# Optimization experiments

Measured on AMD Instinct MI355X. Metric: run time of the kernel, lower is better.

Reference implementation:

```python
import jax, jax.numpy as jnp
import numpy as np
import math

HEADS = 8

def setup_inputs() -> dict:
    key = jax.random.key(0)
    k1, k2 = jax.random.split(key)
    B, C, H, W = 8, 512, 32, 32
    x = jax.random.normal(k1, (B, C, H, W), dtype=jnp.float32)
    # weight-norm 1x1 conv params: v ~ N(0, 0.05), g initialized to ||v|| (torch weight_norm default)
    proj_v = jax.random.normal(k2, (3 * C, C), dtype=jnp.float32) * 0.05
    proj_g = jnp.linalg.norm(proj_v, axis=1)
    proj_b = jnp.zeros((3 * C,), dtype=jnp.float32)
    return {"x": x, "proj_v": proj_v, "proj_g": proj_g, "proj_b": proj_b}

def reference(x, proj_v, proj_g, proj_b):
    B, C, H, W = x.shape
    heads = HEADS
    dim = C // heads
    N = H * W
    # weight-normalized 1x1 conv: w = g * v / ||v|| per output channel
    w = proj_g[:, None] * proj_v / jnp.linalg.norm(proj_v, axis=1, keepdims=True)
    c = jnp.einsum('oc,bchw->bohw', w, x) + proj_b[None, :, None, None]
    c = c.reshape(B, 3, heads, dim, N)
    q, k, v = c[:, 0], c[:, 1], c[:, 2]  # each (B, heads, dim, N)
    scale = 1.0 / math.sqrt(dim)
    attn = jnp.einsum('bhdq,bhdk->bhqk', q, k) * scale  # (B, heads, N, N)
    attn = jax.nn.softmax(attn, axis=-1)
    out = jnp.einsum('bhdk,bhqk->bhdq', v, attn)  # (B, heads, dim, N)
    return x + out.reshape(B, C, H, W)
```

## Files before the change

kernel.cpp:

```cpp
#include <hip/hip_runtime.h>

typedef _Float16 f16;
typedef _Float16 f16x2 __attribute__((ext_vector_type(2)));
typedef _Float16 f16x4 __attribute__((ext_vector_type(4)));
typedef _Float16 f16x8 __attribute__((ext_vector_type(8)));
typedef float f32x4 __attribute__((ext_vector_type(4)));
typedef float f32x16 __attribute__((ext_vector_type(16)));

__device__ inline f32x16 mfma32(f16x8 a, f16x8 b, f32x16 c) {
    return __builtin_amdgcn_mfma_f32_32x32x16_f16(a, b, c, 0, 0, 0);
}

__device__ inline f16x2 pk2(float a, float b) {
    return __builtin_bit_cast(f16x2, __builtin_amdgcn_cvt_pkrtz(a, b));
}

__device__ inline void st8(f16* p, f16x8 v) {
    *(f16x4*)p = __builtin_shufflevector(v, v, 0, 1, 2, 3);
    *(f16x4*)(p + 4) = __builtin_shufflevector(v, v, 4, 5, 6, 7);
}
__device__ inline f16x8 ld8(const f16* p) {
    f16x4 lo = *(const f16x4*)p;
    f16x4 hi = *(const f16x4*)(p + 4);
    return __builtin_shufflevector(lo, hi, 0, 1, 2, 3, 4, 5, 6, 7);
}

__global__ __launch_bounds__(256) void prep_k(const float* __restrict__ pv,
                                              const float* __restrict__ pg,
                                              f16* __restrict__ w,
                                              const float* __restrict__ x,
                                              f16* __restrict__ xT) {
    int bid = blockIdx.x;
    if (bid < 1536) {
        int o = bid;
        const float* row = pv + (size_t)o * 512;
        float s = 0.f;
        for (int c = threadIdx.x; c < 512; c += 256) { float t = row[c]; s += t * t; }
        for (int off = 32; off; off >>= 1) s += __shfl_down(s, off, 64);
        __shared__ float red[4];
        int lane = threadIdx.x & 63, wid = threadIdx.x >> 6;
        if (lane == 0) red[wid] = s;
        __syncthreads();
        float tot = red[0] + red[1] + red[2] + red[3];
        float scale = pg[o] * rsqrtf(tot);
        for (int c = threadIdx.x; c < 512; c += 256)
            w[(size_t)o * 512 + c] = (f16)(row[c] * scale);
    } else {
        int t2 = bid - 1536;
        int n0 = (t2 & 31) * 32, c0 = ((t2 >> 5) & 15) * 32, b = t2 >> 9;
        int tx = threadIdx.x & 31, ty = threadIdx.x >> 5;
        __shared__ float t[32][33];
        const float* xb = x + (size_t)b * 512 * 1024;
        for (int i = 0; i < 4; i++)
            t[ty + 8 * i][tx] = xb[(size_t)(c0 + ty + 8 * i) * 1024 + n0 + tx];
        __syncthreads();
        f16* xTb = xT + (size_t)b * 1024 * 512;
        for (int i = 0; i < 4; i++)
            xTb[(size_t)(n0 + ty + 8 * i) * 512 + c0 + tx] = (f16)t[tx][ty + 8 * i];
    }
}

__global__ __launch_bounds__(256) void qkv_gemm_k(const f16* __restrict__ w,
                                                  const f16* __restrict__ xT,
                                                  const float* __restrict__ pb,
                                                  f16* __restrict__ qk,
                                                  f16* __restrict__ v) {
    __shared__ f16 lA[128 * 64];
    __shared__ f16 lB[128 * 64];
    int b = blockIdx.z;
    int oBase = blockIdx.y * 128;
    int nBase = blockIdx.x * 128;
    const f16* xb = xT + (size_t)b * 1024 * 512;
    int tid = threadIdx.x, lane = tid & 63, warp = tid >> 6;
    int wy = warp >> 1, wx = warp & 1;
    int l31 = lane & 31, hi = lane >> 5;

    int srow = lane >> 3;
    int phys = lane & 7;
    int schunk = phys ^ srow;
    const f16* aS[4]; const f16* bS[4]; int ldsOff[4];
    for (int j = 0; j < 4; j++) {
        int rb = (warp * 4 + j) * 8;
        aS[j] = w  + (size_t)(oBase + rb + srow) * 512 + schunk * 8;
        bS[j] = xb + (size_t)(nBase + rb + srow) * 512 + schunk * 8;
        ldsOff[j] = (rb + srow) * 64 + phys * 8;
    }
    int phk[4];
    for (int ks = 0; ks < 4; ks++)
        phk[ks] = (((ks * 2 + hi) ^ (l31 & 7))) * 8;

    f16x8 rA[4], rB[4];
    for (int j = 0; j < 4; j++) {
        rA[j] = *(const f16x8*)aS[j];
        rB[j] = *(const f16x8*)bS[j];
    }

    f32x16 acc[2][2] = {};

    for (int i = 0; i < 8; i++) {
        __syncthreads();
        for (int j = 0; j < 4; j++) {
            *(f16x8*)&lA[ldsOff[j]] = rA[j];
            *(f16x8*)&lB[ldsOff[j]] = rB[j];
        }
        __syncthreads();
        if (i < 7) {
            int k0 = (i + 1) * 64;
            for (int j = 0; j < 4; j++) {
                rA[j] = *(const f16x8*)(aS[j] + k0);
                rB[j] = *(const f16x8*)(bS[j] + k0);
            }
        }
        for (int ks = 0; ks < 4; ks++) {
            f16x8 af[2], bf[2];
            for (int mi = 0; mi < 2; mi++)
                af[mi] = *(f16x8*)&lA[(wy * 64 + mi * 32 + l31) * 64 + phk[ks]];
            for (int ni = 0; ni < 2; ni++)
                bf[ni] = *(f16x8*)&lB[(wx * 64 + ni * 32 + l31) * 64 + phk[ks]];
            for (int mi = 0; mi < 2; mi++)
                for (int ni = 0; ni < 2; ni++)
                    acc[mi][ni] = mfma32(af[mi], bf[ni], acc[mi][ni]);
        }
    }

    int selB = oBase >> 9;
    for (int mi = 0; mi < 2; mi++) {
        for (int g = 0; g < 4; g++) {
            int oR = oBase + wy * 64 + mi * 32 + 8 * g + 4 * hi;
            int h = (oR >> 6) & 7, d0 = oR & 63;
            for (int ni = 0; ni < 2; ni++) {
                int n = nBase + wx * 64 + ni * 32 + l31;
                if (selB < 2) {
                    float sc = selB == 0 ? 0.125f : 1.0f;
                    f16x4 o4;
                    for (int r = 0; r < 4; r++)
                        o4[r] = (f16)((acc[mi][ni][g * 4 + r] + pb[oR + r]) * sc);
                    *(f16x4*)&qk[((((size_t)b * 2 + selB) * 8 + h) * 1024 + n) * 64 + d0] = o4;
                } else {
                    for (int r = 0; r < 4; r++) {
                        float val = acc[mi][ni][g * 4 + r] + pb[oR + r];
                        v[(((size_t)b * 8 + h) * 64 + d0 + r) * 1024 + n] = (f16)val;
                    }
                }
            }
        }
    }
}

#define ALDK 68
__global__ __launch_bounds__(256) void attn_k(const f16* __restrict__ qk,
                                              const f16* __restrict__ vg,
                                              const float* __restrict__ x,
                                              float* __restrict__ out) {
    __shared__ __align__(16) f16 smem[(2 * 64 + 4 * 32) * ALDK];
    f16* lK = smem;
    f16* lV = smem + 64 * ALDK;
    f16* lPb = smem + 2 * 64 * ALDK;
    float* OT = (float*)smem;

    int bh = blockIdx.y;
    int b = bh >> 3, h = bh & 7;
    int qBase = blockIdx.x * 128;
    int tid = threadIdx.x, lane = tid & 63, warp = tid >> 6;
    int l31 = lane & 31, hi = lane >> 5;

    const f16* qbase = qk + (((size_t)b * 2 + 0) * 8 + h) * 1024 * 64;
    const f16* kbase = qk + (((size_t)b * 2 + 1) * 8 + h) * 1024 * 64;
    const f16* vbase = vg + ((size_t)b * 8 + h) * 64 * 1024;
    f16* lP = lPb + warp * 32 * ALDK;

    int q0 = qBase + warp * 32;
    f16x8 aq[4];
    for (int ks = 0; ks < 4; ks++)
        aq[ks] = *(const f16x8*)&qbase[(size_t)(q0 + l31) * 64 + ks * 16 + hi * 8];

    int sr0 = tid >> 3, sc0 = (tid & 7) * 8;
    int sr1 = (tid + 256) >> 3, sc1 = sc0;

    f16x8 rK[2], rV[2];
    rK[0] = *(const f16x8*)&kbase[(size_t)sr0 * 64 + sc0];
    rK[1] = *(const f16x8*)&kbase[(size_t)sr1 * 64 + sc1];
    rV[0] = *(const f16x8*)&vbase[(size_t)sr0 * 1024 + sc0];
    rV[1] = *(const f16x8*)&vbase[(size_t)sr1 * 1024 + sc1];

    f32x16 accO[2] = {};
    float l_cur = 0.f;

    for (int kt = 0; kt < 16; kt++) {
        __syncthreads();
        st8(&lK[sr0 * ALDK + sc0], rK[0]);
        st8(&lK[sr1 * ALDK + sc1], rK[1]);
        st8(&lV[sr0 * ALDK + sc0], rV[0]);
        st8(&lV[sr1 * ALDK + sc1], rV[1]);
        __syncthreads();
        if (kt < 15) {
            const f16* kb = kbase + (size_t)(kt + 1) * 64 * 64;
            rK[0] = *(const f16x8*)&kb[(size_t)sr0 * 64 + sc0];
            rK[1] = *(const f16x8*)&kb[(size_t)sr1 * 64 + sc1];
            rV[0] = *(const f16x8*)&vbase[(size_t)sr0 * 1024 + (kt + 1) * 64 + sc0];
            rV[1] = *(const f16x8*)&vbase[(size_t)sr1 * 1024 + (kt + 1) * 64 + sc1];
        }

        f32x16 stt[2] = {};
        for (int mt = 0; mt < 2; mt++)
            for (int ks = 0; ks < 4; ks++) {
                f16x8 ak = ld8(&lK[(mt * 32 + l31) * ALDK + ks * 16 + hi * 8]);
                stt[mt] = mfma32(ak, aq[ks], stt[mt]);
            }

        float rs = 0.f;
        for (int mt = 0; mt < 2; mt++)
            for (int g = 0; g < 4; g++) {
                float p0 = __expf(stt[mt][g * 4 + 0]);
                float p1 = __expf(stt[mt][g * 4 + 1]);
                float p2 = __expf(stt[mt][g * 4 + 2]);
                float p3 = __expf(stt[mt][g * 4 + 3]);
                rs += (p0 + p1) + (p2 + p3);
                f16x2 lo = pk2(p0, p1);
                f16x2 hi2 = pk2(p2, p3);
                f16x4 pk;
                pk[0] = lo[0]; pk[1] = lo[1]; pk[2] = hi2[0]; pk[3] = hi2[1];
                *(f16x4*)&lP[l31 * ALDK + mt * 32 + 8 * g + 4 * hi] = pk;
            }
        rs += __shfl_xor(rs, 32, 64);
        l_cur += rs;

        for (int dt = 0; dt < 2; dt++)
            for (int ks = 0; ks < 4; ks++) {
                f16x8 av = ld8(&lV[(dt * 32 + l31) * ALDK + ks * 16 + hi * 8]);
                f16x8 bp = ld8(&lP[l31 * ALDK + ks * 16 + hi * 8]);
                accO[dt] = mfma32(av, bp, accO[dt]);
            }
    }

    __syncthreads();
    float rl = 1.0f / l_cur;
    for (int dt = 0; dt < 2; dt++)
        for (int g = 0; g < 4; g++)
            for (int r = 0; r < 4; r++)
                OT[(dt * 32 + 8 * g + 4 * hi + r) * 132 + warp * 32 + l31] =
                    accO[dt][g * 4 + r] * rl;
    __syncthreads();
    for (int i = 0; i < 8; i++) {
        int cid = tid + 256 * i;
        int d = cid >> 5, qi = (cid & 31) * 4;
        float4 o4 = *(float4*)&OT[d * 132 + qi];
        size_t gi = ((size_t)b * 512 + h * 64 + d) * 1024 + qBase + qi;
        float4 xv = *(const float4*)&x[gi];
        o4.x += xv.x; o4.y += xv.y; o4.z += xv.z; o4.w += xv.w;
        *(float4*)&out[gi] = o4;
    }
}

extern "C" void kernel_launch(void* const* d_in, const int* in_sizes, int n_in,
                              void* d_out, int out_size, void* d_ws, size_t ws_size,
                              hipStream_t stream) {
    (void)in_sizes; (void)n_in; (void)out_size; (void)ws_size;
    const float* x  = (const float*)d_in[0];
    const float* pv = (const float*)d_in[1];
    const float* pg = (const float*)d_in[2];
    const float* pb = (const float*)d_in[3];
    float* out = (float*)d_out;

    char* ws = (char*)d_ws;
    f16* w   = (f16*)(ws);
    f16* xT  = (f16*)(ws + 1572864);
    f16* qk  = (f16*)(ws + 1572864 + 8388608);
    f16* v   = (f16*)(ws + 1572864 + 8388608 + 16777216);

    hipLaunchKernelGGL(prep_k,     dim3(5632),     dim3(256), 0, stream, pv, pg, w, x, xT);
    hipLaunchKernelGGL(qkv_gemm_k, dim3(8, 12, 8), dim3(256), 0, stream, w, xT, pb, qk, v);
    hipLaunchKernelGGL(attn_k,     dim3(8, 64),    dim3(256), 0, stream, qk, v, x, out);
}
```

Baseline: 134.3 us.

## Keep softmax probabilities in registers and double per-warp query tile in attention

The attention kernel now has each warp process 64 queries instead of 32, so every K/V tile loaded into LDS is reused across twice as many queries and the grid halves. The P matrix is no longer staged through shared memory. The packed fp16 exponentials are rearranged into the MFMA B-operand layout with cross-half-wave shuffles. The epilogue writes output directly from registers instead of transposing through LDS. The costs are higher register pressure (launch_bounds set to 1 block), fewer blocks (256) on the device, and uncoalesced strided global stores in the epilogue.

Result: faster. 129.1 us (-3.9%).

```diff
diff --git a/kernel.cpp b/kernel.cpp
--- a/kernel.cpp
+++ b/kernel.cpp
@@ -6,13 +6,15 @@
 typedef _Float16 f16x8 __attribute__((ext_vector_type(8)));
 typedef float f32x4 __attribute__((ext_vector_type(4)));
 typedef float f32x16 __attribute__((ext_vector_type(16)));
+typedef unsigned int u32;
+typedef unsigned int u32x4 __attribute__((ext_vector_type(4)));
 
 __device__ inline f32x16 mfma32(f16x8 a, f16x8 b, f32x16 c) {
     return __builtin_amdgcn_mfma_f32_32x32x16_f16(a, b, c, 0, 0, 0);
 }
 
-__device__ inline f16x2 pk2(float a, float b) {
-    return __builtin_bit_cast(f16x2, __builtin_amdgcn_cvt_pkrtz(a, b));
+__device__ inline u32 pk2u(float a, float b) {
+    return __builtin_bit_cast(u32, __builtin_amdgcn_cvt_pkrtz(a, b));
 }
 
 __device__ inline void st8(f16* p, f16x8 v) {
@@ -148,107 +150,119 @@
 }
 
 #define ALDK 68
-__global__ __launch_bounds__(256) void attn_k(const f16* __restrict__ qk,
-                                              const f16* __restrict__ vg,
-                                              const float* __restrict__ x,
-                                              float* __restrict__ out) {
-    __shared__ __align__(16) f16 smem[(2 * 64 + 4 * 32) * ALDK];
+__global__ __launch_bounds__(256, 1) void attn_k(const f16* __restrict__ qk,
+                                                 const f16* __restrict__ vg,
+                                                 const float* __restrict__ x,
+                                                 float* __restrict__ out) {
+    __shared__ __align__(16) f16 smem[2 * 64 * ALDK];
     f16* lK = smem;
     f16* lV = smem + 64 * ALDK;
-    f16* lPb = smem + 2 * 64 * ALDK;
-    float* OT = (float*)smem;
 
     int bh = blockIdx.y;
     int b = bh >> 3, h = bh & 7;
-    int qBase = blockIdx.x * 128;
+    int qBase = blockIdx.x * 256;
     int tid = threadIdx.x, lane = tid & 63, warp = tid >> 6;
     int l31 = lane & 31, hi = lane >> 5;
 
     const f16* qbase = qk + (((size_t)b * 2 + 0) * 8 + h) * 1024 * 64;
     const f16* kbase = qk + (((size_t)b * 2 + 1) * 8 + h) * 1024 * 64;
     const f16* vbase = vg + ((size_t)b * 8 + h) * 64 * 1024;
-    f16* lP = lPb + warp * 32 * ALDK;
-
-    int q0 = qBase + warp * 32;
-    f16x8 aq[4];
-    for (int ks = 0; ks < 4; ks++)
-        aq[ks] = *(const f16x8*)&qbase[(size_t)(q0 + l31) * 64 + ks * 16 + hi * 8];
+
+    int q0 = qBase + warp * 64;
+    f16x8 aq[2][4];
+    for (int qs = 0; qs < 2; qs++)
+        for (int ks = 0; ks < 4; ks++)
+            aq[qs][ks] = *(const f16x8*)
+                &qbase[(size_t)(q0 + qs * 32 + l31) * 64 + ks * 16 + hi * 8];
 
     int sr0 = tid >> 3, sc0 = (tid & 7) * 8;
-    int sr1 = (tid + 256) >> 3, sc1 = sc0;
+    int sr1 = sr0 + 32;
 
     f16x8 rK[2], rV[2];
     rK[0] = *(const f16x8*)&kbase[(size_t)sr0 * 64 + sc0];
-    rK[1] = *(const f16x8*)&kbase[(size_t)sr1 * 64 + sc1];
+    rK[1] = *(const f16x8*)&kbase[(size_t)sr1 * 64 + sc0];
     rV[0] = *(const f16x8*)&vbase[(size_t)sr0 * 1024 + sc0];
-    rV[1] = *(const f16x8*)&vbase[(size_t)sr1 * 1024 + sc1];
-
-    f32x16 accO[2] = {};
-    float l_cur = 0.f;
+    rV[1] = *(const f16x8*)&vbase[(size_t)sr1 * 1024 + sc0];
+
+    f32x16 accO[2][2] = {};
+    float l_acc[2] = {0.f, 0.f};
 
     for (int kt = 0; kt < 16; kt++) {
         __syncthreads();
         st8(&lK[sr0 * ALDK + sc0], rK[0]);
-        st8(&lK[sr1 * ALDK + sc1], rK[1]);
+        st8(&lK[sr1 * ALDK + sc0], rK[1]);
         st8(&lV[sr0 * ALDK + sc0], rV[0]);
-        st8(&lV[sr1 * ALDK + sc1], rV[1]);
+        st8(&lV[sr1 * ALDK + sc0], rV[1]);
         __syncthreads();
         if (kt < 15) {
             const f16* kb = kbase + (size_t)(kt + 1) * 64 * 64;
             rK[0] = *(const f16x8*)&kb[(size_t)sr0 * 64 + sc0];
-            rK[1] = *(const f16x8*)&kb[(size_t)sr1 * 64 + sc1];
+            rK[1] = *(const f16x8*)&kb[(size_t)sr1 * 64 + sc0];
             rV[0] = *(const f16x8*)&vbase[(size_t)sr0 * 1024 + (kt + 1) * 64 + sc0];
-            rV[1] = *(const f16x8*)&vbase[(size_t)sr1 * 1024 + (kt + 1) * 64 + sc1];
-        }
-
-        f32x16 stt[2] = {};
-        for (int mt = 0; mt < 2; mt++)
+            rV[1] = *(const f16x8*)&vbase[(size_t)sr1 * 1024 + (kt + 1) * 64 + sc0];
+        }
+
+        u32 P0[2][2][4], P1[2][2][4];
+        for (int mt = 0; mt < 2; mt++) {
+            f16x8 ak[4];
+            for (int ks = 0; ks < 4; ks++)
+                ak[ks] = ld8(&lK[(mt * 32 + l31) * ALDK + ks * 16 + hi * 8]);
+            for (int qs = 0; qs < 2; qs++) {
+                f32x16 stt = {};
+                for (int ks = 0; ks < 4; ks++)
+                    stt = mfma32(ak[ks], aq[qs][ks], stt);
+                float rs = 0.f;
+                for (int g = 0; g < 4; g++) {
+                    float p0 = __expf(stt[g * 4 + 0]);
+                    float p1 = __expf(stt[g * 4 + 1]);
+                    float p2 = __expf(stt[g * 4 + 2]);
+                    float p3 = __expf(stt[g * 4 + 3]);
+                    rs += (p0 + p1) + (p2 + p3);
+                    P0[mt][qs][g] = pk2u(p0, p1);
+                    P1[mt][qs][g] = pk2u(p2, p3);
+                }
+                l_acc[qs] += rs;
+            }
+        }
+
+        f16x8 av[2][4];
+        for (int dt = 0; dt < 2; dt++)
+            for (int ks = 0; ks < 4; ks++)
+                av[dt][ks] = ld8(&lV[(dt * 32 + l31) * ALDK + ks * 16 + hi * 8]);
+        for (int qs = 0; qs < 2; qs++) {
+            f16x8 bfrag[4];
             for (int ks = 0; ks < 4; ks++) {
-                f16x8 ak = ld8(&lK[(mt * 32 + l31) * ALDK + ks * 16 + hi * 8]);
-                stt[mt] = mfma32(ak, aq[ks], stt[mt]);
-            }
-
-        float rs = 0.f;
-        for (int mt = 0; mt < 2; mt++)
-            for (int g = 0; g < 4; g++) {
-                float p0 = __expf(stt[mt][g * 4 + 0]);
-                float p1 = __expf(stt[mt][g * 4 + 1]);
-                float p2 = __expf(stt[mt][g * 4 + 2]);
-                float p3 = __expf(stt[mt][g * 4 + 3]);
-                rs += (p0 + p1) + (p2 + p3);
-                f16x2 lo = pk2(p0, p1);
-                f16x2 hi2 = pk2(p2, p3);
-                f16x4 pk;
-                pk[0] = lo[0]; pk[1] = lo[1]; pk[2] = hi2[0]; pk[3] = hi2[1];
-                *(f16x4*)&lP[l31 * ALDK + mt * 32 + 8 * g + 4 * hi] = pk;
-            }
-        rs += __shfl_xor(rs, 32, 64);
-        l_cur += rs;
-
+                int mt = ks >> 1, ge = 2 * (ks & 1);
+                u32 e00 = P0[mt][qs][ge], e01 = P0[mt][qs][ge + 1];
+                u32 e10 = P1[mt][qs][ge], e11 = P1[mt][qs][ge + 1];
+                u32 k0 = hi ? e01 : e00;
+                u32 k1 = hi ? e11 : e10;
+                u32 s0 = hi ? e00 : e01;
+                u32 s1 = hi ? e10 : e11;
+                u32 r0 = __shfl_xor(s0, 32, 64);
+                u32 r1 = __shfl_xor(s1, 32, 64);
+                u32 a0 = hi ? r0 : k0, a1 = hi ? r1 : k1;
+                u32 b0 = hi ? k0 : r0, b1 = hi ? k1 : r1;
+                u32x4 t = {a0, a1, b0, b1};
+                bfrag[ks] = __builtin_bit_cast(f16x8, t);
+            }
+            for (int dt = 0; dt < 2; dt++)
+                for (int ks = 0; ks < 4; ks++)
+                    accO[dt][qs] = mfma32(av[dt][ks], bfrag[ks], accO[dt][qs]);
+        }
+    }
+
+    for (int qs = 0; qs < 2; qs++) {
+        float lt = l_acc[qs] + __shfl_xor(l_acc[qs], 32, 64);
+        float rl = 1.0f / lt;
+        int q = q0 + qs * 32 + l31;
         for (int dt = 0; dt < 2; dt++)
-            for (int ks = 0; ks < 4; ks++) {
-                f16x8 av = ld8(&lV[(dt * 32 + l31) * ALDK + ks * 16 + hi * 8]);
-                f16x8 bp = ld8(&lP[l31 * ALDK + ks * 16 + hi * 8]);
-                accO[dt] = mfma32(av, bp, accO[dt]);
-            }
-    }
-
-    __syncthreads();
-    float rl = 1.0f / l_cur;
-    for (int dt = 0; dt < 2; dt++)
-        for (int g = 0; g < 4; g++)
-            for (int r = 0; r < 4; r++)
-                OT[(dt * 32 + 8 * g + 4 * hi + r) * 132 + warp * 32 + l31] =
-                    accO[dt][g * 4 + r] * rl;
-    __syncthreads();
-    for (int i = 0; i < 8; i++) {
-        int cid = tid + 256 * i;
-        int d = cid >> 5, qi = (cid & 31) * 4;
-        float4 o4 = *(float4*)&OT[d * 132 + qi];
-        size_t gi = ((size_t)b * 512 + h * 64 + d) * 1024 + qBase + qi;
-        float4 xv = *(const float4*)&x[gi];
-        o4.x += xv.x; o4.y += xv.y; o4.z += xv.z; o4.w += xv.w;
-        *(float4*)&out[gi] = o4;
+            for (int g = 0; g < 4; g++)
+                for (int r = 0; r < 4; r++) {
+                    int d = dt * 32 + 8 * g + 4 * hi + r;
+                    size_t gi = ((size_t)b * 512 + h * 64 + d) * 1024 + q;
+                    out[gi] = x[gi] + accO[dt][qs][g * 4 + r] * rl;
+                }
     }
 }
 
@@ -270,5 +284,5 @@
 
     hipLaunchKernelGGL(prep_k,     dim3(5632),     dim3(256), 0, stream, pv, pg, w, x, xT);
     hipLaunchKernelGGL(qkv_gemm_k, dim3(8, 12, 8), dim3(256), 0, stream, w, xT, pb, qk, v);
-    hipLaunchKernelGGL(attn_k,     dim3(8, 64),    dim3(256), 0, stream, qk, v, x, out);
-}
+    hipLaunchKernelGGL(attn_k,     dim3(4, 64),    dim3(256), 0, stream, qk, v, x, out);
+}
```
